# Kernel tuning notes

Measured on AMD Instinct MI355X. Metric: run time of the kernel, lower is better.

Reference implementation:

```python
import jax, jax.numpy as jnp
import numpy as np

N = 100_000      # nodes
E = 1_600_000    # edges (avg degree 16)
D_IN = 256
D_OUT = 128


def setup_inputs() -> dict:
    key = jax.random.key(0)
    ks = jax.random.split(key, 13)
    stdv = 1.0 / np.sqrt(D_OUT)      # matches reset_parameters
    std_att = 1.0                    # att_vec_* have fan 1 -> stdv 1
    std_av = 1.0 / np.sqrt(3.0)
    return {
        "x": jax.random.normal(ks[0], (N, D_IN), dtype=jnp.float32),
        "edge_src": jax.random.randint(ks[1], (E,), 0, N),
        "edge_dst": jax.random.randint(ks[2], (E,), 0, N),
        "w_low": jax.random.uniform(ks[3], (E,), dtype=jnp.float32) / 16.0,   # ~normalized adj
        "w_high": jax.random.normal(ks[4], (E,), dtype=jnp.float32) / 16.0,    # high-pass weights can be +/-
        "w_unnorm": jax.random.uniform(ks[5], (E,), dtype=jnp.float32),
        "W_low": jax.random.uniform(ks[6], (D_IN, D_OUT), jnp.float32, -stdv, stdv),
        "W_high": jax.random.uniform(ks[7], (D_IN, D_OUT), jnp.float32, -stdv, stdv),
        "W_mlp": jax.random.uniform(ks[8], (D_IN, D_OUT), jnp.float32, -stdv, stdv),
        "a_low": jax.random.uniform(ks[9], (D_OUT, 1), jnp.float32, -std_att, std_att),
        "a_high": jax.random.uniform(ks[10], (D_OUT, 1), jnp.float32, -std_att, std_att),
        "a_mlp": jax.random.uniform(ks[11], (D_OUT, 1), jnp.float32, -std_att, std_att),
        "att_vec": jax.random.uniform(ks[12], (3, 3), jnp.float32, -std_av, std_av),
    }


def _spmm(w, src, dst, h, n):
    # sparse [n,n] @ dense [n,d]: gather source rows, weight, scatter-add to dest
    return jax.ops.segment_sum(w[:, None] * h[src], dst, num_segments=n)


def reference(x, edge_src, edge_dst, w_low, w_high, w_unnorm,
              W_low, W_high, W_mlp, a_low, a_high, a_mlp, att_vec):
    n = x.shape[0]
    # variant=False path: relu(spmm(adj, x @ W))
    h_low = jax.nn.relu(_spmm(w_low, edge_src, edge_dst, x @ W_low, n))
    h_high = jax.nn.relu(_spmm(w_high, edge_src, edge_dst, x @ W_high, n))
    h_mlp = jax.nn.relu(x @ W_mlp)
    # attention3: sigmoid of per-branch scalar scores -> 3x3 mix -> softmax (T=3)
    scores = jnp.concatenate([h_low @ a_low, h_high @ a_high, h_mlp @ a_mlp], axis=1)  # [n,3]
    att = jax.nn.softmax((jax.nn.sigmoid(scores) @ att_vec) / 3.0, axis=1)
    return 3.0 * (att[:, 0:1] * h_low + att[:, 1:2] * h_high + att[:, 2:3] * h_mlp)
```

## Files before the change

### kernel.cpp

```cpp
#include <hip/hip_runtime.h>
#include <hip/hip_bf16.h>
#include <math.h>

#define D_IN   256
#define D_OUT  128
#define DZ     384
#define NHB    256

typedef __attribute__((ext_vector_type(8))) short short8;
typedef __attribute__((ext_vector_type(4))) float floatx4;

__device__ __forceinline__ unsigned short f2bf(float f) {
  union { float f; unsigned u; } v; v.f = f;
  unsigned r = v.u + 0x7fffu + ((v.u >> 16) & 1u);
  return (unsigned short)(r >> 16);
}

__global__ __launch_bounds__(256) void hist_prep_kernel(
    const float* __restrict__ Wl, const float* __restrict__ Wh,
    const float* __restrict__ Wm, unsigned short* __restrict__ Bpack,
    const float* __restrict__ x, unsigned short* __restrict__ xb, int n8,
    const int* __restrict__ dst, int* __restrict__ bh, int E, int NB1) {
  __shared__ int hist[1024];
  const int bid = blockIdx.x;
  const int t = threadIdx.x;
  if (bid < NHB) {
    for (int k = t; k < NB1; k += 256) hist[k] = 0;
    __syncthreads();
    const int chunk = (E + NHB - 1) / NHB;
    const int base = bid * chunk;
    const int lim = min(E, base + chunk);
    for (int e = base + t; e < lim; e += 256) atomicAdd(&hist[dst[e] >> 7], 1);
    __syncthreads();
    for (int k = t; k < NB1; k += 256) bh[k * NHB + bid] = hist[k];
  } else if (bid < NHB + 384) {
    int tt = (bid - NHB) * 256 + t;
    int j = tt & 7;
    int lane = (tt >> 3) & 63;
    int f = tt >> 9;
    int nt = f % 24, kt = f / 24;
    int k = kt * 32 + (lane >> 4) * 8 + j;
    int n_ = nt * 16 + (lane & 15);
    const float* W = (n_ < 128) ? Wl : (n_ < 256 ? Wh : Wm);
    Bpack[tt] = f2bf(W[k * D_OUT + (n_ & 127)]);
  } else {
    int i = (bid - NHB - 384) * 256 + t;
    if (i < n8) {
      const float4* p = (const float4*)x + (size_t)i * 2;
      float4 f0 = p[0], f1 = p[1];
      short8 o;
      o[0] = (short)f2bf(f0.x); o[1] = (short)f2bf(f0.y);
      o[2] = (short)f2bf(f0.z); o[3] = (short)f2bf(f0.w);
      o[4] = (short)f2bf(f1.x); o[5] = (short)f2bf(f1.y);
      o[6] = (short)f2bf(f1.z); o[7] = (short)f2bf(f1.w);
      ((short8*)xb)[i] = o;
    }
  }
}

__global__ __launch_bounds__(256) void scan1_kernel(
    const int* __restrict__ cnt, int* __restrict__ outp,
    int* __restrict__ bsum, int n) {
  __shared__ int sd[256];
  int t = threadIdx.x;
  int base = blockIdx.x * 1024 + t * 4;
  int v0 = base + 0 < n ? cnt[base + 0] : 0;
  int v1 = base + 1 < n ? cnt[base + 1] : 0;
  int v2 = base + 2 < n ? cnt[base + 2] : 0;
  int v3 = base + 3 < n ? cnt[base + 3] : 0;
  int tsum = v0 + v1 + v2 + v3;
  sd[t] = tsum;
  __syncthreads();
  for (int off = 1; off < 256; off <<= 1) {
    int add = (t >= off) ? sd[t - off] : 0;
    __syncthreads();
    sd[t] += add;
    __syncthreads();
  }
  int excl = sd[t] - tsum;
  if (base + 0 < n) outp[base + 0] = excl;
  if (base + 1 < n) outp[base + 1] = excl + v0;
  if (base + 2 < n) outp[base + 2] = excl + v0 + v1;
  if (base + 3 < n) outp[base + 3] = excl + v0 + v1 + v2;
  if (t == 255) bsum[blockIdx.x] = sd[255];
}

__global__ __launch_bounds__(256) void scan2_kernel(int* __restrict__ bsum,
                                                    int nb) {
  __shared__ int sd[256];
  int t = threadIdx.x;
  int v = t < nb ? bsum[t] : 0;
  sd[t] = v;
  __syncthreads();
  for (int off = 1; off < 256; off <<= 1) {
    int add = (t >= off) ? sd[t - off] : 0;
    __syncthreads();
    sd[t] += add;
    __syncthreads();
  }
  if (t < nb) bsum[t] = sd[t] - v;
}

__global__ void scan3_kernel(int* __restrict__ outp,
                             const int* __restrict__ bsum, int n) {
  int i = blockIdx.x * 256 + threadIdx.x;
  if (i < n) outp[i] += bsum[i >> 10];
}

#define LDSROW 392
__global__ __launch_bounds__(512, 4) void gemm_sort_kernel(
    const unsigned short* __restrict__ xb,
    const unsigned short* __restrict__ Bpack, unsigned short* __restrict__ Z,
    int n_nodes, const int* __restrict__ src, const int* __restrict__ dst,
    const float* __restrict__ wlo, const float* __restrict__ whi,
    const int* __restrict__ bhscan, uint2* __restrict__ tmp, int E, int NB1) {
  __shared__ unsigned short tile[64 * LDSROW];
  const int bid = blockIdx.x;

  int gemm_id;
  if (bid < 2 * NHB) {
    if ((bid & 1) == 0) {
      int rb = bid >> 1;
      int* cur = (int*)tile;
      int t = threadIdx.x;
      for (int k = t; k < NB1; k += 512) cur[k] = bhscan[k * NHB + rb];
      __syncthreads();
      const int chunk = (E + NHB - 1) / NHB;
      const int base = rb * chunk;
      const int lim = min(E, base + chunk);
      for (int e = base + t; e < lim; e += 512) {
        int d = dst[e];
        int pos = atomicAdd(&cur[d >> 7], 1);
        unsigned wl = f2bf(wlo[e]), wh = f2bf(whi[e]);
        tmp[pos] = make_uint2((unsigned)src[e] | ((unsigned)(d & 127) << 20),
                              wl | (wh << 16));
      }
      return;
    }
    gemm_id = bid >> 1;
  } else {
    gemm_id = bid - 2 * NHB + NHB;
  }

  const int lane = threadIdx.x & 63;
  const int w = threadIdx.x >> 6;
  const int rowbase = gemm_id * 64;
  const int m16 = lane & 15, quad = lane >> 4;

  floatx4 acc[4][3];
#pragma unroll
  for (int s = 0; s < 4; s++)
#pragma unroll
    for (int c = 0; c < 3; c++) acc[s][c] = (floatx4)(0.f);

  const short8* xr[4];
#pragma unroll
  for (int s = 0; s < 4; s++) {
    int r = rowbase + s * 16 + m16;
    if (r > n_nodes - 1) r = n_nodes - 1;
    xr[s] = (const short8*)xb + (size_t)r * 32 + quad;
  }
  const short8* bp = (const short8*)Bpack + lane;

#pragma unroll
  for (int kt = 0; kt < 8; kt++) {
    short8 a[4];
#pragma unroll
    for (int s = 0; s < 4; s++) a[s] = xr[s][kt * 4];
#pragma unroll
    for (int c = 0; c < 3; c++) {
      short8 b = bp[(kt * 24 + w * 3 + c) * 64];
#pragma unroll
      for (int s = 0; s < 4; s++)
        acc[s][c] =
            __builtin_amdgcn_mfma_f32_16x16x32_bf16(a[s], b, acc[s][c], 0, 0, 0);
    }
  }

#pragma unroll
  for (int s = 0; s < 4; s++)
#pragma unroll
    for (int c = 0; c < 3; c++)
#pragma unroll
      for (int r = 0; r < 4; r++)
        tile[(s * 16 + quad * 4 + r) * LDSROW + (w * 3 + c) * 16 + m16] =
            f2bf(acc[s][c][r]);
  __syncthreads();

#pragma unroll
  for (int it = 0; it < 6; it++) {
    int chunk = it * 512 + threadIdx.x;
    int row = chunk / 48, col = (chunk % 48) * 8;
    int grow = rowbase + row;
    if (grow < n_nodes)
      *(short8*)(Z + (size_t)grow * DZ + col) =
          *(const short8*)&tile[row * LDSROW + col];
  }
}

__global__ __launch_bounds__(256) void fine_kernel(
    const uint2* __restrict__ tmp, const int* __restrict__ bhscan,
    uint2* __restrict__ meta, int* __restrict__ rowptr, int NB1, int n, int E) {
  __shared__ int fh[128];
  __shared__ int sd[128];
  __shared__ int cur[128];
  const int b = blockIdx.x;
  const int t = threadIdx.x;
  const int s0 = bhscan[b * NHB];
  const int s1 = (b == NB1 - 1) ? E : bhscan[(b + 1) * NHB];

  if (t < 128) fh[t] = 0;
  __syncthreads();
  for (int i = s0 + t; i < s1; i += 256)
    atomicAdd(&fh[(tmp[i].x >> 20) & 127], 1);
  __syncthreads();

  if (t < 128) sd[t] = fh[t];
  __syncthreads();
  for (int off = 1; off < 128; off <<= 1) {
    int add = (t >= off && t < 128) ? sd[t - off] : 0;
    __syncthreads();
    if (t < 128) sd[t] += add;
    __syncthreads();
  }
  if (t < 128) {
    int excl = sd[t] - fh[t];
    cur[t] = excl;
    int node = b * 128 + t;
    if (node < n) rowptr[node] = s0 + excl;
  }
  if (b == 0 && t == 0) rowptr[n] = E;
  __syncthreads();

  for (int i = s0 + t; i < s1; i += 256) {
    uint2 v = tmp[i];
    int d = (v.x >> 20) & 127;
    int pos = s0 + atomicAdd(&cur[d], 1);
    meta[pos] = make_uint2(v.x & 0xFFFFFu, v.y);
  }
}

__global__ __launch_bounds__(128) void node_kernel(
    const unsigned short* __restrict__ Zh, const int* __restrict__ rowptr,
    const uint2* __restrict__ meta, const float* __restrict__ a_low,
    const float* __restrict__ a_high, const float* __restrict__ a_mlp,
    const float* __restrict__ att_vec, float* __restrict__ out, int n_nodes) {
  int node = blockIdx.x * 2 + (threadIdx.x >> 6);
  if (node >= n_nodes) return;
  node = __builtin_amdgcn_readfirstlane(node);
  const int lane = threadIdx.x & 63;
  const int isHigh = lane >> 5;
  const int dbase = (lane & 31) * 4;
  const char* Zb = (const char*)Zh;

  const int start = rowptr[node];
  const int end = rowptr[node + 1];

  float acc0 = 0.f, acc1 = 0.f, acc2 = 0.f, acc3 = 0.f;
  auto wsel = [&](unsigned p) {
    return __uint_as_float(isHigh ? (p & 0xffff0000u) : (p << 16));
  };
  auto step = [&](uint2 z, float wv) {
    acc0 += wv * __uint_as_float(z.x << 16);
    acc1 += wv * __uint_as_float(z.x & 0xffff0000u);
    acc2 += wv * __uint_as_float(z.y << 16);
    acc3 += wv * __uint_as_float(z.y & 0xffff0000u);
  };

  int j = start;
  const int nfull = (end - start) & ~7;
  for (; j < start + nfull; j += 8) {
    uint2 m[8], z[8];
#pragma unroll
    for (int u = 0; u < 8; u++) m[u] = meta[j + u];
#pragma unroll
    for (int u = 0; u < 8; u++)
      z[u] = *(const uint2*)(Zb + (size_t)m[u].x * 768 + lane * 8);
#pragma unroll
    for (int u = 0; u < 8; u++) step(z[u], wsel(m[u].y));
  }
  for (; j < end; j++) {
    uint2 m0 = meta[j];
    uint2 z0 = *(const uint2*)(Zb + (size_t)m0.x * 768 + lane * 8);
    step(z0, wsel(m0.y));
  }

  float h0 = fmaxf(acc0, 0.f), h1 = fmaxf(acc1, 0.f);
  float h2 = fmaxf(acc2, 0.f), h3 = fmaxf(acc3, 0.f);

  uint2 zm =
      *(const uint2*)(Zb + (size_t)node * 768 + 512 + (size_t)(lane & 31) * 8);
  float q0 = fmaxf(__uint_as_float(zm.x << 16), 0.f);
  float q1 = fmaxf(__uint_as_float(zm.x & 0xffff0000u), 0.f);
  float q2 = fmaxf(__uint_as_float(zm.y << 16), 0.f);
  float q3 = fmaxf(__uint_as_float(zm.y & 0xffff0000u), 0.f);

  const float* av_b = isHigh ? a_high : a_low;
  float4 ab = *(const float4*)&av_b[dbase];
  float4 am = *(const float4*)&a_mlp[dbase];
  float v1 = h0 * ab.x + h1 * ab.y + h2 * ab.z + h3 * ab.w;
  float v2 = isHigh ? 0.f : (q0 * am.x + q1 * am.y + q2 * am.z + q3 * am.w);
#pragma unroll
  for (int off = 1; off < 32; off <<= 1) {
    v1 += __shfl_xor(v1, off);
    v2 += __shfl_xor(v2, off);
  }
  float s_lo = __shfl(v1, 0);
  float s_hi = __shfl(v1, 32);
  float s_ml = __shfl(v2, 0);

  float g0 = 1.f / (1.f + __expf(-s_lo));
  float g1 = 1.f / (1.f + __expf(-s_hi));
  float g2 = 1.f / (1.f + __expf(-s_ml));
  const float inv3 = 1.f / 3.f;
  float m0 = (g0 * att_vec[0] + g1 * att_vec[3] + g2 * att_vec[6]) * inv3;
  float m1 = (g0 * att_vec[1] + g1 * att_vec[4] + g2 * att_vec[7]) * inv3;
  float m2 = (g0 * att_vec[2] + g1 * att_vec[5] + g2 * att_vec[8]) * inv3;
  float mx = fmaxf(m0, fmaxf(m1, m2));
  float e0 = __expf(m0 - mx), e1 = __expf(m1 - mx), e2 = __expf(m2 - mx);
  float inv = 1.f / (e0 + e1 + e2);
  float c0 = 3.f * inv * e0, c1 = 3.f * inv * e1, c2 = 3.f * inv * e2;

  float hh0 = __shfl_xor(h0, 32);
  float hh1 = __shfl_xor(h1, 32);
  float hh2 = __shfl_xor(h2, 32);
  float hh3 = __shfl_xor(h3, 32);

  if (!isHigh) {
    float4 o;
    o.x = c0 * h0 + c1 * hh0 + c2 * q0;
    o.y = c0 * h1 + c1 * hh1 + c2 * q1;
    o.z = c0 * h2 + c1 * hh2 + c2 * q2;
    o.w = c0 * h3 + c1 * hh3 + c2 * q3;
    *(float4*)&out[(size_t)node * D_OUT + dbase] = o;
  }
}

extern "C" void kernel_launch(void* const* d_in, const int* in_sizes, int n_in,
                              void* d_out, int out_size, void* d_ws,
                              size_t ws_size, hipStream_t stream) {
  const float* x    = (const float*)d_in[0];
  const int*   esrc = (const int*)d_in[1];
  const int*   edst = (const int*)d_in[2];
  const float* wlo  = (const float*)d_in[3];
  const float* whi  = (const float*)d_in[4];
  const float* Wl   = (const float*)d_in[6];
  const float* Wh   = (const float*)d_in[7];
  const float* Wm   = (const float*)d_in[8];
  const float* alo  = (const float*)d_in[9];
  const float* ahi  = (const float*)d_in[10];
  const float* amlp = (const float*)d_in[11];
  const float* av   = (const float*)d_in[12];
  float* out = (float*)d_out;

  const int N = in_sizes[0] / D_IN;
  const int E = in_sizes[1];
  const int NB1 = (N + 127) >> 7;
  const int M = NB1 * NHB;

  char* ws = (char*)d_ws;
  size_t off = 0;
  auto carve = [&](size_t bytes) -> void* {
    void* p = ws + off;
    off = (off + bytes + 255) & ~(size_t)255;
    return p;
  };
  unsigned short* Z      = (unsigned short*)carve((size_t)N * DZ * 2);
  unsigned short* xb     = (unsigned short*)carve((size_t)N * D_IN * 2);
  unsigned short* Bpack  = (unsigned short*)carve(98304 * 2);
  int*   bh     = (int*)carve((size_t)M * 4);
  int*   bhscan = (int*)carve((size_t)M * 4);
  int*   bsum   = (int*)carve(256 * 4);
  int*   rowptr = (int*)carve((size_t)(N + 1) * 4);
  uint2* tmp    = (uint2*)carve((size_t)E * 8);
  uint2* meta   = (uint2*)carve((size_t)E * 8);

  int n8 = in_sizes[0] / 8;
  int nxb = (n8 + 255) / 256;

  hist_prep_kernel<<<NHB + 384 + nxb, 256, 0, stream>>>(Wl, Wh, Wm, Bpack, x,
                                                        xb, n8, edst, bh, E,
                                                        NB1);
  int nb1s = (M + 1023) / 1024;
  scan1_kernel<<<nb1s, 256, 0, stream>>>(bh, bhscan, bsum, M);
  scan2_kernel<<<1, 256, 0, stream>>>(bsum, nb1s);
  scan3_kernel<<<(M + 255) / 256, 256, 0, stream>>>(bhscan, bsum, M);

  int ngemm = (N + 63) / 64;
  gemm_sort_kernel<<<ngemm + NHB, 512, 0, stream>>>(
      xb, Bpack, Z, N, esrc, edst, wlo, whi, bhscan, tmp, E, NB1);

  fine_kernel<<<NB1, 256, 0, stream>>>(tmp, bhscan, meta, rowptr, NB1, N, E);

  node_kernel<<<(N + 1) / 2, 128, 0, stream>>>(Z, rowptr, meta, alo, ahi, amlp,
                                               av, out, N);
}
```

Baseline: 451.2 us.

## Fold scan3 into consumers, halve GEMM LDS tile, double-buffer gather loop

Removes the scan3 kernel launch by adding the block-sum offset at the point where bhscan is read in the sort and fine kernels. The GEMM epilogue now stages output through a half-size LDS tile in two passes, and launch bounds are raised to allow more resident blocks. The node kernel's edge gather loop is software-pipelined with two register buffers of eight edges each so loads for the next group overlap the FMAs of the current one. The extra register pressure may reduce occupancy, and the two-pass epilogue adds a barrier.

```diff
diff --git a/kernel.cpp b/kernel.cpp
--- a/kernel.cpp
+++ b/kernel.cpp
@@ -101,20 +101,15 @@
   if (t < nb) bsum[t] = sd[t] - v;
 }
 
-__global__ void scan3_kernel(int* __restrict__ outp,
-                             const int* __restrict__ bsum, int n) {
-  int i = blockIdx.x * 256 + threadIdx.x;
-  if (i < n) outp[i] += bsum[i >> 10];
-}
-
 #define LDSROW 392
-__global__ __launch_bounds__(512, 4) void gemm_sort_kernel(
+__global__ __launch_bounds__(512, 8) void gemm_sort_kernel(
     const unsigned short* __restrict__ xb,
     const unsigned short* __restrict__ Bpack, unsigned short* __restrict__ Z,
     int n_nodes, const int* __restrict__ src, const int* __restrict__ dst,
     const float* __restrict__ wlo, const float* __restrict__ whi,
-    const int* __restrict__ bhscan, uint2* __restrict__ tmp, int E, int NB1) {
-  __shared__ unsigned short tile[64 * LDSROW];
+    const int* __restrict__ bhscan, const int* __restrict__ bsum,
+    uint2* __restrict__ tmp, int E, int NB1) {
+  __shared__ unsigned short tile[32 * LDSROW];
   const int bid = blockIdx.x;
 
   int gemm_id;
@@ -123,7 +118,10 @@
       int rb = bid >> 1;
       int* cur = (int*)tile;
       int t = threadIdx.x;
-      for (int k = t; k < NB1; k += 512) cur[k] = bhscan[k * NHB + rb];
+      for (int k = t; k < NB1; k += 512) {
+        int idx = k * NHB + rb;
+        cur[k] = bhscan[idx] + bsum[idx >> 10];
+      }
       __syncthreads();
       const int chunk = (E + NHB - 1) / NHB;
       const int base = rb * chunk;
@@ -178,36 +176,41 @@
   }
 
 #pragma unroll
-  for (int s = 0; s < 4; s++)
-#pragma unroll
-    for (int c = 0; c < 3; c++)
-#pragma unroll
-      for (int r = 0; r < 4; r++)
-        tile[(s * 16 + quad * 4 + r) * LDSROW + (w * 3 + c) * 16 + m16] =
-            f2bf(acc[s][c][r]);
-  __syncthreads();
-
-#pragma unroll
-  for (int it = 0; it < 6; it++) {
-    int chunk = it * 512 + threadIdx.x;
-    int row = chunk / 48, col = (chunk % 48) * 8;
-    int grow = rowbase + row;
-    if (grow < n_nodes)
-      *(short8*)(Z + (size_t)grow * DZ + col) =
-          *(const short8*)&tile[row * LDSROW + col];
+  for (int half = 0; half < 2; half++) {
+    if (half) __syncthreads();
+#pragma unroll
+    for (int s = 0; s < 2; s++)
+#pragma unroll
+      for (int c = 0; c < 3; c++)
+#pragma unroll
+        for (int r = 0; r < 4; r++)
+          tile[(s * 16 + quad * 4 + r) * LDSROW + (w * 3 + c) * 16 + m16] =
+              f2bf(acc[half * 2 + s][c][r]);
+    __syncthreads();
+#pragma unroll
+    for (int it = 0; it < 3; it++) {
+      int chunk = it * 512 + threadIdx.x;
+      int row = chunk / 48, col = (chunk % 48) * 8;
+      int grow = rowbase + half * 32 + row;
+      if (grow < n_nodes)
+        *(short8*)(Z + (size_t)grow * DZ + col) =
+            *(const short8*)&tile[row * LDSROW + col];
+    }
   }
 }
 
 __global__ __launch_bounds__(256) void fine_kernel(
     const uint2* __restrict__ tmp, const int* __restrict__ bhscan,
-    uint2* __restrict__ meta, int* __restrict__ rowptr, int NB1, int n, int E) {
+    const int* __restrict__ bsum, uint2* __restrict__ meta,
+    int* __restrict__ rowptr, int NB1, int n, int E) {
   __shared__ int fh[128];
   __shared__ int sd[128];
   __shared__ int cur[128];
   const int b = blockIdx.x;
   const int t = threadIdx.x;
-  const int s0 = bhscan[b * NHB];
-  const int s1 = (b == NB1 - 1) ? E : bhscan[(b + 1) * NHB];
+  auto scanidx = [&](int i) { return bhscan[i] + bsum[i >> 10]; };
+  const int s0 = scanidx(b * NHB);
+  const int s1 = (b == NB1 - 1) ? E : scanidx((b + 1) * NHB);
 
   if (t < 128) fh[t] = 0;
   __syncthreads();
@@ -267,19 +270,32 @@
     acc3 += wv * __uint_as_float(z.y & 0xffff0000u);
   };
 
-  int j = start;
-  const int nfull = (end - start) & ~7;
-  for (; j < start + nfull; j += 8) {
-    uint2 m[8], z[8];
-#pragma unroll
-    for (int u = 0; u < 8; u++) m[u] = meta[j + u];
+  uint2 mA[8], zA[8], mB[8], zB[8];
+  auto loadg = [&](uint2* m, uint2* z, int g) {
+    int jj = start + g * 8;
+#pragma unroll
+    for (int u = 0; u < 8; u++) m[u] = meta[jj + u];
 #pragma unroll
     for (int u = 0; u < 8; u++)
       z[u] = *(const uint2*)(Zb + (size_t)m[u].x * 768 + lane * 8);
+  };
+  auto computeg = [&](const uint2* m, const uint2* z) {
 #pragma unroll
     for (int u = 0; u < 8; u++) step(z[u], wsel(m[u].y));
-  }
-  for (; j < end; j++) {
+  };
+
+  const int n8cnt = (end - start) >> 3;
+  if (n8cnt > 0) loadg(mA, zA, 0);
+  if (n8cnt > 1) loadg(mB, zB, 1);
+  int g = 0;
+  for (; g + 1 < n8cnt; g += 2) {
+    computeg(mA, zA);
+    if (g + 2 < n8cnt) loadg(mA, zA, g + 2);
+    computeg(mB, zB);
+    if (g + 3 < n8cnt) loadg(mB, zB, g + 3);
+  }
+  if (g < n8cnt) computeg(mA, zA);
+  for (int j = start + n8cnt * 8; j < end; j++) {
     uint2 m0 = meta[j];
     uint2 z0 = *(const uint2*)(Zb + (size_t)m0.x * 768 + lane * 8);
     step(z0, wsel(m0.y));
@@ -384,13 +400,13 @@
   int nb1s = (M + 1023) / 1024;
   scan1_kernel<<<nb1s, 256, 0, stream>>>(bh, bhscan, bsum, M);
   scan2_kernel<<<1, 256, 0, stream>>>(bsum, nb1s);
-  scan3_kernel<<<(M + 255) / 256, 256, 0, stream>>>(bhscan, bsum, M);
 
   int ngemm = (N + 63) / 64;
   gemm_sort_kernel<<<ngemm + NHB, 512, 0, stream>>>(
-      xb, Bpack, Z, N, esrc, edst, wlo, whi, bhscan, tmp, E, NB1);
-
-  fine_kernel<<<NB1, 256, 0, stream>>>(tmp, bhscan, meta, rowptr, NB1, N, E);
+      xb, Bpack, Z, N, esrc, edst, wlo, whi, bhscan, bsum, tmp, E, NB1);
+
+  fine_kernel<<<NB1, 256, 0, stream>>>(tmp, bhscan, bsum, meta, rowptr, NB1, N,
+                                       E);
 
   node_kernel<<<(N + 1) / 2, 128, 0, stream>>>(Z, rowptr, meta, alo, ahi, amlp,
                                                av, out, N);
```

New measurement: 586.4 us. 30.0% more time.
